# Kernel tuning notes

Measured on AMD Instinct MI355X. Metric: run time of the kernel, lower is better.

Reference implementation:

```python
import jax, jax.numpy as jnp
import numpy as np

B, T, H, OUT = 128, 1024, 256, 2


def setup_inputs() -> dict:
    key = jax.random.key(0)
    ks = jax.random.split(key, 16)
    s_in = 1.0 / np.sqrt(1 + H)
    s_2h = 1.0 / np.sqrt(2 * H)
    s_o = 1.0 / np.sqrt(H)
    return {
        "x": jax.random.normal(ks[0], (B, T, 2), dtype=jnp.float32),
        "h_0": jax.random.normal(ks[1], (1, B, H), dtype=jnp.float32) * 0.1,
        "Wa": jax.random.normal(ks[2], (1 + H, H), dtype=jnp.float32) * s_in,
        "ba": jnp.zeros((H,), dtype=jnp.float32),
        "Wp1": jax.random.normal(ks[3], (1 + H, H), dtype=jnp.float32) * s_in,
        "bp1": jnp.zeros((H,), dtype=jnp.float32),
        "Wp2": jax.random.normal(ks[4], (1 + H, H), dtype=jnp.float32) * s_in,
        "bp2": jnp.zeros((H,), dtype=jnp.float32),
        "Wz": jax.random.normal(ks[5], (2 * H, H), dtype=jnp.float32) * s_2h,
        "bz": jnp.zeros((H,), dtype=jnp.float32),
        "Wh": jax.random.normal(ks[6], (2 * H, H), dtype=jnp.float32) * s_2h,
        "bh": jnp.zeros((H,), dtype=jnp.float32),
        "Wo": jax.random.normal(ks[7], (H, OUT), dtype=jnp.float32) * s_o,
        "bo": jnp.zeros((OUT,), dtype=jnp.float32),
    }


def _pgjanet_scan(x, h0, Wa, ba, Wp1, bp1, Wp2, bp2, Wz, bz, Wh, bh):
    # x: [B, T, 2], h0: [B, H]
    xt_all = jnp.swapaxes(x, 0, 1)  # [T, B, 2]

    def step(h, xt):
        amp = xt[:, 0:1]                       # [B, 1]
        ph = xt[:, 1:2]                        # [B, 1]
        a = jnp.tanh(jnp.concatenate([amp, h], axis=-1) @ Wa + ba)
        p1 = jnp.tanh(jnp.concatenate([jnp.cos(ph), h], axis=-1) @ Wp1 + bp1)
        p2 = jnp.tanh(jnp.concatenate([jnp.sin(ph), h], axis=-1) @ Wp2 + bp2)
        u = a * p1 * p2 * (1 - a) * (1 - p1) * (1 - p2)
        newin = jnp.concatenate([u, h], axis=-1)  # [B, 2H]
        z = jax.nn.sigmoid(newin @ Wz + bz)
        h_cand = jnp.tanh(newin @ Wh + bh)
        h_new = z * h + (1 - z) * h_cand
        return h_new, h_new

    h_n, hs = jax.lax.scan(step, h0, xt_all)
    return jnp.swapaxes(hs, 0, 1), h_n  # [B, T, H], [B, H]


def reference(x, h_0, Wa, ba, Wp1, bp1, Wp2, bp2, Wz, bz, Wh, bh, Wo, bo):
    hs, h_n = _pgjanet_scan(x, h_0[0], Wa, ba, Wp1, bp1, Wp2, bp2, Wz, bz, Wh, bh)
    out = hs @ Wo + bo  # [B, T, OUT]
    return (out, h_n)
```

## Files before the change

kernel.cpp:

```cpp
#include <hip/hip_runtime.h>
#include <math.h>


#define B_   128
#define T_   1024
#define H_   256
#define GB   32
#define GC   8
#define MB   4
#define NS   32
#define NTHR 512
#define HP   260

typedef float    f32x4 __attribute__((ext_vector_type(4)));
typedef unsigned u32x4 __attribute__((ext_vector_type(4)));

__device__ __forceinline__ void sys_st_x4(unsigned* p, u32x4 v) {
  asm volatile("global_store_dwordx4 %0, %1, off sc0 sc1" :: "v"(p), "v"(v) : "memory");
}
__device__ __forceinline__ u32x4 sys_ld_x4(const unsigned* p) {
  u32x4 v;
  asm volatile("global_load_dwordx4 %0, %1, off sc0 sc1\n\ts_waitcnt vmcnt(0)"
               : "=v"(v) : "v"(p) : "memory");
  return v;
}

__launch_bounds__(NTHR, 1)
__global__ void pgjanet_persist(
    const float* __restrict__ x,   const float* __restrict__ h0,
    const float* __restrict__ Wa,  const float* __restrict__ ba,
    const float* __restrict__ Wp1, const float* __restrict__ bp1,
    const float* __restrict__ Wp2, const float* __restrict__ bp2,
    const float* __restrict__ Wz,  const float* __restrict__ bz,
    const float* __restrict__ Wh,  const float* __restrict__ bh,
    const float* __restrict__ Wo,  const float* __restrict__ bo,
    float* __restrict__ out,
    unsigned* __restrict__ u_ex,
    unsigned* __restrict__ h_ex)
{
  __shared__ __align__(16) float h_lds[MB][HP];
  __shared__ __align__(16) float u_lds[MB][HP];
  __shared__ __align__(16) float wo_s[H_ * 2];
  __shared__ __align__(16) float xin[2][MB][4];

  const int wg   = blockIdx.x;
  const int g    = wg >> 3;
  const int gc   = wg & 7;
  const int tid  = threadIdx.x;
  const int col  = tid >> 4;
  const int kk   = tid & 15;
  const int b0   = g * MB;
  const int colg = gc * NS + col;

  f32x4 w1r[3][4]; float w1r0_[3], b1_[3];
#pragma unroll
  for (int m = 0; m < 3; ++m) {
    const float* W  = (m == 0) ? Wa : (m == 1 ? Wp1 : Wp2);
    const float* bb = (m == 0) ? ba : (m == 1 ? bp1 : bp2);
#pragma unroll
    for (int j = 0; j < 4; ++j) {
      f32x4 w;
#pragma unroll
      for (int c = 0; c < 4; ++c)
        w[c] = W[(1 + kk * 4 + j * 64 + c) * H_ + colg];
      w1r[m][j] = w;
    }
    w1r0_[m] = W[colg];
    b1_[m]   = bb[colg];
  }
  f32x4 w2r[2][8];
#pragma unroll
  for (int m = 0; m < 2; ++m) {
    const float* W = (m == 0) ? Wz : Wh;
#pragma unroll
    for (int j = 0; j < 8; ++j) {
      int rb = (j < 4) ? (kk * 4 + j * 64) : (256 + kk * 4 + (j - 4) * 64);
      f32x4 w;
#pragma unroll
      for (int c = 0; c < 4; ++c)
        w[c] = W[(rb + c) * H_ + colg];
      w2r[m][j] = w;
    }
  }
  const float bz_c = bz[colg], bh_c = bh[colg];
  const float bo0 = bo[0], bo1 = bo[1];
  for (int i = tid; i < H_ * 2; i += NTHR) wo_s[i] = Wo[i];
  {
    int b = tid >> 7, c2 = (tid & 127) * 2;
    float2 hv = *(const float2*)(h0 + (size_t)(b0 + b) * H_ + c2);
    h_lds[b][c2] = hv.x; h_lds[b][c2 + 1] = hv.y;
  }
  if (tid < MB) {
    float2 xt = *(const float2*)(x + ((size_t)(b0 + tid) * T_) * 2);
    xin[0][tid][0] = xt.x; xin[0][tid][1] = cosf(xt.y);
    xin[0][tid][2] = sinf(xt.y); xin[0][tid][3] = 0.f;
  }
  __syncthreads();

  unsigned* u_exg = u_ex + g * 2048;
  unsigned* h_exg = h_ex + g * 2048;
  unsigned* u_my  = u_exg + (gc * 64 + (col >> 1) * 4) * 4;
  unsigned* h_my  = h_exg + (gc * 64 + (col >> 1) * 4) * 4;
  const unsigned* pu = u_exg + tid * 4;
  const unsigned* ph = h_exg + tid * 4;
  const int cpg = ((tid >> 6) * 16 + ((tid >> 2) & 15)) * 2;
  const int cb  = tid & 3;
  const int em  = kk >> 2, eb = kk & 3;

  for (int t = 0; t < T_; ++t) {
    const unsigned seq = (unsigned)(t + 1);
    const int xb = t & 1;

    float acc[12];
#pragma unroll
    for (int i = 0; i < 12; ++i) acc[i] = 0.f;
#pragma unroll
    for (int b = 0; b < MB; ++b) {
#pragma unroll
      for (int j = 0; j < 4; ++j) {
        f32x4 h4 = *(const f32x4*)&h_lds[b][kk * 4 + j * 64];
#pragma unroll
        for (int m = 0; m < 3; ++m) {
          float s = acc[m * 4 + b];
          s = fmaf(h4[0], w1r[m][j][0], s); s = fmaf(h4[1], w1r[m][j][1], s);
          s = fmaf(h4[2], w1r[m][j][2], s); s = fmaf(h4[3], w1r[m][j][3], s);
          acc[m * 4 + b] = s;
        }
      }
    }
#pragma unroll
    for (int i = 0; i < 12; ++i) {
      float v = acc[i];
      v += __shfl_xor(v, 1); v += __shfl_xor(v, 2);
      v += __shfl_xor(v, 4); v += __shfl_xor(v, 8);
      acc[i] = v;
    }
    {
      float pre1 = acc[0];
#pragma unroll
      for (int i = 1; i < 12; ++i) if (kk == i) pre1 = acc[i];
      float w0  = em == 0 ? w1r0_[0] : (em == 1 ? w1r0_[1] : w1r0_[2]);
      float bb1 = em == 0 ? b1_[0]   : (em == 1 ? b1_[1]   : b1_[2]);
      f32x4 xi4 = *(const f32x4*)&xin[xb][eb][0];
      float xim = em == 0 ? xi4[0] : (em == 1 ? xi4[1] : xi4[2]);
      float tv  = tanhf(pre1 + xim * w0 + bb1);
      float p1v = __shfl(tv, kk + 4, 16);
      float p2v = __shfl(tv, kk + 8, 16);
      float uv  = tv * p1v * p2v * (1.f - tv) * (1.f - p1v) * (1.f - p2v);
      float uodd = __shfl_xor(uv, 16);
      if (kk < 4 && !(col & 1)) {
        u32x4 ch;
        ch.x = __float_as_uint(uv); ch.y = __float_as_uint(uodd);
        ch.z = seq; ch.w = 0u;
        sys_st_x4(u_my + eb * 4, ch);
      }
    }

    float acc2[8];
#pragma unroll
    for (int i = 0; i < 8; ++i) acc2[i] = 0.f;
#pragma unroll
    for (int b = 0; b < MB; ++b) {
#pragma unroll
      for (int j = 0; j < 4; ++j) {
        f32x4 h4 = *(const f32x4*)&h_lds[b][kk * 4 + j * 64];
#pragma unroll
        for (int m = 0; m < 2; ++m) {
          float s = acc2[m * 4 + b];
          s = fmaf(h4[0], w2r[m][4 + j][0], s); s = fmaf(h4[1], w2r[m][4 + j][1], s);
          s = fmaf(h4[2], w2r[m][4 + j][2], s); s = fmaf(h4[3], w2r[m][4 + j][3], s);
          acc2[m * 4 + b] = s;
        }
      }
    }

    {
      u32x4 c;
      for (;;) {
        c = sys_ld_x4(pu);
        if (c.z == seq) break;
        __builtin_amdgcn_s_sleep(1);
      }
      float2 d; d.x = __uint_as_float(c.x); d.y = __uint_as_float(c.y);
      *(float2*)&u_lds[cb][cpg] = d;
    }
    __syncthreads();

#pragma unroll
    for (int b = 0; b < MB; ++b) {
#pragma unroll
      for (int j = 0; j < 4; ++j) {
        f32x4 u4 = *(const f32x4*)&u_lds[b][kk * 4 + j * 64];
#pragma unroll
        for (int m = 0; m < 2; ++m) {
          float s = acc2[m * 4 + b];
          s = fmaf(u4[0], w2r[m][j][0], s); s = fmaf(u4[1], w2r[m][j][1], s);
          s = fmaf(u4[2], w2r[m][j][2], s); s = fmaf(u4[3], w2r[m][j][3], s);
          acc2[m * 4 + b] = s;
        }
      }
    }
#pragma unroll
    for (int i = 0; i < 8; ++i) {
      float v = acc2[i];
      v += __shfl_xor(v, 1); v += __shfl_xor(v, 2);
      v += __shfl_xor(v, 4); v += __shfl_xor(v, 8);
      acc2[i] = v;
    }
    {
      float pre2 = acc2[0];
#pragma unroll
      for (int i = 1; i < 8; ++i) if (kk == i) pre2 = acc2[i];
      float v2 = pre2 + (em == 0 ? bz_c : bh_c);
      float gv;
      if (em == 0) gv = 1.f / (1.f + expf(-v2));
      else         gv = tanhf(v2);
      float hcv   = __shfl(gv, kk + 4, 16);
      float hprev = h_lds[eb][colg];
      float hn    = gv * hprev + (1.f - gv) * hcv;
      float hnodd = __shfl_xor(hn, 16);
      if (kk < 4 && !(col & 1)) {
        u32x4 ch;
        ch.x = __float_as_uint(hn); ch.y = __float_as_uint(hnodd);
        ch.z = seq; ch.w = 0u;
        sys_st_x4(h_my + eb * 4, ch);
      }
      if (t == T_ - 1 && kk < 4)
        out[(size_t)B_ * T_ * 2 + (size_t)(b0 + eb) * H_ + colg] = hn;
    }

    if (t > 0 && gc < MB && tid < 64) {
      f32x4 h4  = *(const f32x4*)&h_lds[gc][tid * 4];
      f32x4 wo0 = *(const f32x4*)&wo_s[tid * 8];
      f32x4 wo1 = *(const f32x4*)&wo_s[tid * 8 + 4];
      float v0 = h4[0] * wo0[0] + h4[1] * wo0[2] + h4[2] * wo1[0] + h4[3] * wo1[2];
      float v1 = h4[0] * wo0[1] + h4[1] * wo0[3] + h4[2] * wo1[1] + h4[3] * wo1[3];
      v0 += __shfl_xor(v0, 1);  v1 += __shfl_xor(v1, 1);
      v0 += __shfl_xor(v0, 2);  v1 += __shfl_xor(v1, 2);
      v0 += __shfl_xor(v0, 4);  v1 += __shfl_xor(v1, 4);
      v0 += __shfl_xor(v0, 8);  v1 += __shfl_xor(v1, 8);
      v0 += __shfl_xor(v0, 16); v1 += __shfl_xor(v1, 16);
      v0 += __shfl_xor(v0, 32); v1 += __shfl_xor(v1, 32);
      if (tid == 0) {
        float2 o; o.x = v0 + bo0; o.y = v1 + bo1;
        *(float2*)(out + ((size_t)(b0 + gc) * T_ + (t - 1)) * 2) = o;
      }
    }
    if (t + 1 < T_ && tid < MB) {
      float2 xt = *(const float2*)(x + ((size_t)(b0 + tid) * T_ + (t + 1)) * 2);
      xin[xb ^ 1][tid][0] = xt.x; xin[xb ^ 1][tid][1] = cosf(xt.y);
      xin[xb ^ 1][tid][2] = sinf(xt.y); xin[xb ^ 1][tid][3] = 0.f;
    }
    __syncthreads();

    {
      u32x4 c;
      for (;;) {
        c = sys_ld_x4(ph);
        if (c.z == seq) break;
        __builtin_amdgcn_s_sleep(1);
      }
      float2 d; d.x = __uint_as_float(c.x); d.y = __uint_as_float(c.y);
      *(float2*)&h_lds[cb][cpg] = d;
    }
    __syncthreads();
  }

  if (gc < MB && tid < 64) {
    f32x4 h4  = *(const f32x4*)&h_lds[gc][tid * 4];
    f32x4 wo0 = *(const f32x4*)&wo_s[tid * 8];
    f32x4 wo1 = *(const f32x4*)&wo_s[tid * 8 + 4];
    float v0 = h4[0] * wo0[0] + h4[1] * wo0[2] + h4[2] * wo1[0] + h4[3] * wo1[2];
    float v1 = h4[0] * wo0[1] + h4[1] * wo0[3] + h4[2] * wo1[1] + h4[3] * wo1[3];
    v0 += __shfl_xor(v0, 1);  v1 += __shfl_xor(v1, 1);
    v0 += __shfl_xor(v0, 2);  v1 += __shfl_xor(v1, 2);
    v0 += __shfl_xor(v0, 4);  v1 += __shfl_xor(v1, 4);
    v0 += __shfl_xor(v0, 8);  v1 += __shfl_xor(v1, 8);
    v0 += __shfl_xor(v0, 16); v1 += __shfl_xor(v1, 16);
    v0 += __shfl_xor(v0, 32); v1 += __shfl_xor(v1, 32);
    if (tid == 0) {
      float2 o; o.x = v0 + bo0; o.y = v1 + bo1;
      *(float2*)(out + ((size_t)(b0 + gc) * T_ + (T_ - 1)) * 2) = o;
    }
  }
}

extern "C" void kernel_launch(void* const* d_in, const int* in_sizes, int n_in,
                              void* d_out, int out_size, void* d_ws, size_t ws_size,
                              hipStream_t stream) {
  (void)in_sizes; (void)n_in; (void)out_size; (void)ws_size;
  const float* x   = (const float*)d_in[0];
  const float* h0  = (const float*)d_in[1];
  const float* Wa  = (const float*)d_in[2];
  const float* ba  = (const float*)d_in[3];
  const float* Wp1 = (const float*)d_in[4];
  const float* bp1 = (const float*)d_in[5];
  const float* Wp2 = (const float*)d_in[6];
  const float* bp2 = (const float*)d_in[7];
  const float* Wz  = (const float*)d_in[8];
  const float* bz  = (const float*)d_in[9];
  const float* Wh  = (const float*)d_in[10];
  const float* bh  = (const float*)d_in[11];
  const float* Wo  = (const float*)d_in[12];
  const float* bo  = (const float*)d_in[13];

  float* out = (float*)d_out;
  char*  ws  = (char*)d_ws;
  unsigned* u_ex = (unsigned*)ws;
  unsigned* h_ex = (unsigned*)(ws + 262144);

  hipMemsetAsync(ws, 0, 524288, stream);

  pgjanet_persist<<<dim3(GB * GC), dim3(NTHR), 0, stream>>>(
      x, h0, Wa, ba, Wp1, bp1, Wp2, bp2, Wz, bz, Wh, bh, Wo, bo,
      out, u_ex, h_ex);
}
```

Baseline: 6.948 ms.

## Repartition persistent GRU across 16 groups of 8 batches with 16 column-split blocks

```diff
diff --git a/kernel.cpp b/kernel.cpp
--- a/kernel.cpp
+++ b/kernel.cpp
@@ -5,12 +5,11 @@
 #define B_   128
 #define T_   1024
 #define H_   256
-#define GB   32
-#define GC   8
-#define MB   4
-#define NS   32
+#define GB   16
+#define GC   16
+#define MB   8
 #define NTHR 512
-#define HP   260
+#define HPAD 264
 
 typedef float    f32x4 __attribute__((ext_vector_type(4)));
 typedef unsigned u32x4 __attribute__((ext_vector_type(4)));
@@ -18,11 +17,12 @@
 __device__ __forceinline__ void sys_st_x4(unsigned* p, u32x4 v) {
   asm volatile("global_store_dwordx4 %0, %1, off sc0 sc1" :: "v"(p), "v"(v) : "memory");
 }
-__device__ __forceinline__ u32x4 sys_ld_x4(const unsigned* p) {
-  u32x4 v;
-  asm volatile("global_load_dwordx4 %0, %1, off sc0 sc1\n\ts_waitcnt vmcnt(0)"
-               : "=v"(v) : "v"(p) : "memory");
-  return v;
+__device__ __forceinline__ void sys_ld2_x4(const unsigned* p0, const unsigned* p1,
+                                           u32x4& a, u32x4& b) {
+  asm volatile("global_load_dwordx4 %0, %2, off sc0 sc1\n\t"
+               "global_load_dwordx4 %1, %3, off sc0 sc1\n\t"
+               "s_waitcnt vmcnt(0)"
+               : "=&v"(a), "=&v"(b) : "v"(p0), "v"(p1) : "memory");
 }
 
 __launch_bounds__(NTHR, 1)
@@ -38,19 +38,23 @@
     unsigned* __restrict__ u_ex,
     unsigned* __restrict__ h_ex)
 {
-  __shared__ __align__(16) float h_lds[MB][HP];
-  __shared__ __align__(16) float u_lds[MB][HP];
+  __shared__ __align__(16) float h_lds[MB * HPAD];
+  __shared__ __align__(16) float u_lds[MB * HPAD];
   __shared__ __align__(16) float wo_s[H_ * 2];
   __shared__ __align__(16) float xin[2][MB][4];
 
   const int wg   = blockIdx.x;
-  const int g    = wg >> 3;
-  const int gc   = wg & 7;
+  const int g    = wg >> 4;
+  const int gc   = wg & 15;
   const int tid  = threadIdx.x;
-  const int col  = tid >> 4;
-  const int kk   = tid & 15;
+  const int lane = tid & 63;
+  const int w    = tid >> 6;
+  const int kl   = lane & 15;
+  const int bhlf = (lane >> 4) & 1;
+  const int cp   = (lane >> 5) & 1;
+  const int col  = w * 2 + cp;
+  const int colg = gc * 16 + col;
   const int b0   = g * MB;
-  const int colg = gc * NS + col;
 
   f32x4 w1r[3][4]; float w1r0_[3], b1_[3];
 #pragma unroll
@@ -59,11 +63,11 @@
     const float* bb = (m == 0) ? ba : (m == 1 ? bp1 : bp2);
 #pragma unroll
     for (int j = 0; j < 4; ++j) {
-      f32x4 w;
+      f32x4 v;
 #pragma unroll
       for (int c = 0; c < 4; ++c)
-        w[c] = W[(1 + kk * 4 + j * 64 + c) * H_ + colg];
-      w1r[m][j] = w;
+        v[c] = W[(1 + kl * 4 + j * 64 + c) * H_ + colg];
+      w1r[m][j] = v;
     }
     w1r0_[m] = W[colg];
     b1_[m]   = bb[colg];
@@ -74,21 +78,21 @@
     const float* W = (m == 0) ? Wz : Wh;
 #pragma unroll
     for (int j = 0; j < 8; ++j) {
-      int rb = (j < 4) ? (kk * 4 + j * 64) : (256 + kk * 4 + (j - 4) * 64);
-      f32x4 w;
+      int rb = (j < 4) ? (kl * 4 + j * 64) : (256 + kl * 4 + (j - 4) * 64);
+      f32x4 v;
 #pragma unroll
       for (int c = 0; c < 4; ++c)
-        w[c] = W[(rb + c) * H_ + colg];
-      w2r[m][j] = w;
+        v[c] = W[(rb + c) * H_ + colg];
+      w2r[m][j] = v;
     }
   }
   const float bz_c = bz[colg], bh_c = bh[colg];
   const float bo0 = bo[0], bo1 = bo[1];
   for (int i = tid; i < H_ * 2; i += NTHR) wo_s[i] = Wo[i];
   {
-    int b = tid >> 7, c2 = (tid & 127) * 2;
-    float2 hv = *(const float2*)(h0 + (size_t)(b0 + b) * H_ + c2);
-    h_lds[b][c2] = hv.x; h_lds[b][c2 + 1] = hv.y;
+    int row = tid >> 6, k4 = (tid & 63) * 4;
+    *(f32x4*)&h_lds[row * HPAD + k4] =
+        *(const f32x4*)(h0 + (size_t)(b0 + row) * H_ + k4);
   }
   if (tid < MB) {
     float2 xt = *(const float2*)(x + ((size_t)(b0 + tid) * T_) * 2);
@@ -97,15 +101,14 @@
   }
   __syncthreads();
 
-  unsigned* u_exg = u_ex + g * 2048;
-  unsigned* h_exg = h_ex + g * 2048;
-  unsigned* u_my  = u_exg + (gc * 64 + (col >> 1) * 4) * 4;
-  unsigned* h_my  = h_exg + (gc * 64 + (col >> 1) * 4) * 4;
-  const unsigned* pu = u_exg + tid * 4;
-  const unsigned* ph = h_exg + tid * 4;
-  const int cpg = ((tid >> 6) * 16 + ((tid >> 2) & 15)) * 2;
-  const int cb  = tid & 3;
-  const int em  = kk >> 2, eb = kk & 3;
+  unsigned* u_exg = u_ex + g * 4096;
+  unsigned* h_exg = h_ex + g * 4096;
+  unsigned* u_my  = u_exg + ((gc * 8 + w) * 8) * 4;
+  unsigned* h_my  = h_exg + ((gc * 8 + w) * 8) * 4;
+  const unsigned* pu0 = u_exg + tid * 4;
+  const unsigned* pu1 = u_exg + (tid + 512) * 4;
+  const unsigned* ph0 = h_exg + tid * 4;
+  const unsigned* ph1 = h_exg + (tid + 512) * 4;
 
   for (int t = 0; t < T_; ++t) {
     const unsigned seq = (unsigned)(t + 1);
@@ -115,16 +118,17 @@
 #pragma unroll
     for (int i = 0; i < 12; ++i) acc[i] = 0.f;
 #pragma unroll
-    for (int b = 0; b < MB; ++b) {
+    for (int bb = 0; bb < 4; ++bb) {
+      const float* hr = &h_lds[(bhlf * 4 + bb) * HPAD];
 #pragma unroll
       for (int j = 0; j < 4; ++j) {
-        f32x4 h4 = *(const f32x4*)&h_lds[b][kk * 4 + j * 64];
+        f32x4 h4 = *(const f32x4*)(hr + kl * 4 + j * 64);
 #pragma unroll
         for (int m = 0; m < 3; ++m) {
-          float s = acc[m * 4 + b];
+          float s = acc[m * 4 + bb];
           s = fmaf(h4[0], w1r[m][j][0], s); s = fmaf(h4[1], w1r[m][j][1], s);
           s = fmaf(h4[2], w1r[m][j][2], s); s = fmaf(h4[3], w1r[m][j][3], s);
-          acc[m * 4 + b] = s;
+          acc[m * 4 + bb] = s;
         }
       }
     }
@@ -137,102 +141,40 @@
     }
     {
       float pre1 = acc[0];
-#pragma unroll
-      for (int i = 1; i < 12; ++i) if (kk == i) pre1 = acc[i];
-      float w0  = em == 0 ? w1r0_[0] : (em == 1 ? w1r0_[1] : w1r0_[2]);
-      float bb1 = em == 0 ? b1_[0]   : (em == 1 ? b1_[1]   : b1_[2]);
-      f32x4 xi4 = *(const f32x4*)&xin[xb][eb][0];
-      float xim = em == 0 ? xi4[0] : (em == 1 ? xi4[1] : xi4[2]);
+      pre1 = (kl == 1)  ? acc[1]  : pre1;  pre1 = (kl == 2)  ? acc[2]  : pre1;
+      pre1 = (kl == 3)  ? acc[3]  : pre1;  pre1 = (kl == 4)  ? acc[4]  : pre1;
+      pre1 = (kl == 5)  ? acc[5]  : pre1;  pre1 = (kl == 6)  ? acc[6]  : pre1;
+      pre1 = (kl == 7)  ? acc[7]  : pre1;  pre1 = (kl == 8)  ? acc[8]  : pre1;
+      pre1 = (kl == 9)  ? acc[9]  : pre1;  pre1 = (kl == 10) ? acc[10] : pre1;
+      pre1 = (kl == 11) ? acc[11] : pre1;
+      int m = kl >> 2;
+      int batch = bhlf * 4 + (kl & 3);
+      float w0  = (m == 0) ? w1r0_[0] : ((m == 1) ? w1r0_[1] : w1r0_[2]);
+      float bb1 = (m == 0) ? b1_[0]   : ((m == 1) ? b1_[1]   : b1_[2]);
+      float xam = xin[xb][batch][0], xcs = xin[xb][batch][1], xsn = xin[xb][batch][2];
+      float xim = (m == 0) ? xam : ((m == 1) ? xcs : xsn);
       float tv  = tanhf(pre1 + xim * w0 + bb1);
-      float p1v = __shfl(tv, kk + 4, 16);
-      float p2v = __shfl(tv, kk + 8, 16);
+      float p1v = __shfl(tv, kl + 4, 16);
+      float p2v = __shfl(tv, kl + 8, 16);
       float uv  = tv * p1v * p2v * (1.f - tv) * (1.f - p1v) * (1.f - p2v);
-      float uodd = __shfl_xor(uv, 16);
-      if (kk < 4 && !(col & 1)) {
+      float uodd = __shfl_xor(uv, 32);
+      if (lane < 32 && kl < 4) {
         u32x4 ch;
         ch.x = __float_as_uint(uv); ch.y = __float_as_uint(uodd);
         ch.z = seq; ch.w = 0u;
-        sys_st_x4(u_my + eb * 4, ch);
-      }
-    }
-
-    float acc2[8];
-#pragma unroll
-    for (int i = 0; i < 8; ++i) acc2[i] = 0.f;
-#pragma unroll
-    for (int b = 0; b < MB; ++b) {
-#pragma unroll
-      for (int j = 0; j < 4; ++j) {
-        f32x4 h4 = *(const f32x4*)&h_lds[b][kk * 4 + j * 64];
-#pragma unroll
-        for (int m = 0; m < 2; ++m) {
-          float s = acc2[m * 4 + b];
-          s = fmaf(h4[0], w2r[m][4 + j][0], s); s = fmaf(h4[1], w2r[m][4 + j][1], s);
-          s = fmaf(h4[2], w2r[m][4 + j][2], s); s = fmaf(h4[3], w2r[m][4 + j][3], s);
-          acc2[m * 4 + b] = s;
-        }
-      }
-    }
-
-    {
-      u32x4 c;
-      for (;;) {
-        c = sys_ld_x4(pu);
-        if (c.z == seq) break;
-        __builtin_amdgcn_s_sleep(1);
-      }
-      float2 d; d.x = __uint_as_float(c.x); d.y = __uint_as_float(c.y);
-      *(float2*)&u_lds[cb][cpg] = d;
-    }
-    __syncthreads();
-
-#pragma unroll
-    for (int b = 0; b < MB; ++b) {
-#pragma unroll
-      for (int j = 0; j < 4; ++j) {
-        f32x4 u4 = *(const f32x4*)&u_lds[b][kk * 4 + j * 64];
-#pragma unroll
-        for (int m = 0; m < 2; ++m) {
-          float s = acc2[m * 4 + b];
-          s = fmaf(u4[0], w2r[m][j][0], s); s = fmaf(u4[1], w2r[m][j][1], s);
-          s = fmaf(u4[2], w2r[m][j][2], s); s = fmaf(u4[3], w2r[m][j][3], s);
-          acc2[m * 4 + b] = s;
-        }
-      }
-    }
-#pragma unroll
-    for (int i = 0; i < 8; ++i) {
-      float v = acc2[i];
-      v += __shfl_xor(v, 1); v += __shfl_xor(v, 2);
-      v += __shfl_xor(v, 4); v += __shfl_xor(v, 8);
-      acc2[i] = v;
-    }
-    {
-      float pre2 = acc2[0];
-#pragma unroll
-      for (int i = 1; i < 8; ++i) if (kk == i) pre2 = acc2[i];
-      float v2 = pre2 + (em == 0 ? bz_c : bh_c);
-      float gv;
-      if (em == 0) gv = 1.f / (1.f + expf(-v2));
-      else         gv = tanhf(v2);
-      float hcv   = __shfl(gv, kk + 4, 16);
-      float hprev = h_lds[eb][colg];
-      float hn    = gv * hprev + (1.f - gv) * hcv;
-      float hnodd = __shfl_xor(hn, 16);
-      if (kk < 4 && !(col & 1)) {
-        u32x4 ch;
-        ch.x = __float_as_uint(hn); ch.y = __float_as_uint(hnodd);
-        ch.z = seq; ch.w = 0u;
-        sys_st_x4(h_my + eb * 4, ch);
-      }
-      if (t == T_ - 1 && kk < 4)
-        out[(size_t)B_ * T_ * 2 + (size_t)(b0 + eb) * H_ + colg] = hn;
-    }
-
-    if (t > 0 && gc < MB && tid < 64) {
-      f32x4 h4  = *(const f32x4*)&h_lds[gc][tid * 4];
-      f32x4 wo0 = *(const f32x4*)&wo_s[tid * 8];
-      f32x4 wo1 = *(const f32x4*)&wo_s[tid * 8 + 4];
+        sys_st_x4(u_my + (bhlf * 4 + kl) * 4, ch);
+      }
+    }
+
+    if (t + 1 < T_ && tid < MB) {
+      float2 xt = *(const float2*)(x + ((size_t)(b0 + tid) * T_ + (t + 1)) * 2);
+      xin[xb ^ 1][tid][0] = xt.x; xin[xb ^ 1][tid][1] = cosf(xt.y);
+      xin[xb ^ 1][tid][2] = sinf(xt.y); xin[xb ^ 1][tid][3] = 0.f;
+    }
+    if (t > 0 && ((t - 1) & 15) == gc) {
+      f32x4 h4  = *(const f32x4*)&h_lds[w * HPAD + lane * 4];
+      f32x4 wo0 = *(const f32x4*)&wo_s[lane * 8];
+      f32x4 wo1 = *(const f32x4*)&wo_s[lane * 8 + 4];
       float v0 = h4[0] * wo0[0] + h4[1] * wo0[2] + h4[2] * wo1[0] + h4[3] * wo1[2];
       float v1 = h4[0] * wo0[1] + h4[1] * wo0[3] + h4[2] * wo1[1] + h4[3] * wo1[3];
       v0 += __shfl_xor(v0, 1);  v1 += __shfl_xor(v1, 1);
@@ -241,35 +183,114 @@
       v0 += __shfl_xor(v0, 8);  v1 += __shfl_xor(v1, 8);
       v0 += __shfl_xor(v0, 16); v1 += __shfl_xor(v1, 16);
       v0 += __shfl_xor(v0, 32); v1 += __shfl_xor(v1, 32);
-      if (tid == 0) {
+      if (lane == 0) {
         float2 o; o.x = v0 + bo0; o.y = v1 + bo1;
-        *(float2*)(out + ((size_t)(b0 + gc) * T_ + (t - 1)) * 2) = o;
-      }
-    }
-    if (t + 1 < T_ && tid < MB) {
-      float2 xt = *(const float2*)(x + ((size_t)(b0 + tid) * T_ + (t + 1)) * 2);
-      xin[xb ^ 1][tid][0] = xt.x; xin[xb ^ 1][tid][1] = cosf(xt.y);
-      xin[xb ^ 1][tid][2] = sinf(xt.y); xin[xb ^ 1][tid][3] = 0.f;
+        *(float2*)(out + ((size_t)(b0 + w) * T_ + (t - 1)) * 2) = o;
+      }
+    }
+    float acc2[8];
+#pragma unroll
+    for (int i = 0; i < 8; ++i) acc2[i] = 0.f;
+#pragma unroll
+    for (int bb = 0; bb < 4; ++bb) {
+      const float* hr = &h_lds[(bhlf * 4 + bb) * HPAD];
+#pragma unroll
+      for (int j = 0; j < 4; ++j) {
+        f32x4 h4 = *(const f32x4*)(hr + kl * 4 + j * 64);
+#pragma unroll
+        for (int m = 0; m < 2; ++m) {
+          float s = acc2[m * 4 + bb];
+          s = fmaf(h4[0], w2r[m][4 + j][0], s); s = fmaf(h4[1], w2r[m][4 + j][1], s);
+          s = fmaf(h4[2], w2r[m][4 + j][2], s); s = fmaf(h4[3], w2r[m][4 + j][3], s);
+          acc2[m * 4 + bb] = s;
+        }
+      }
+    }
+
+    {
+      u32x4 A, Bc;
+      for (;;) {
+        sys_ld2_x4(pu0, pu1, A, Bc);
+        if (A.z == seq && Bc.z == seq) break;
+        __builtin_amdgcn_s_sleep(1);
+      }
+      int c = tid;
+      float2 d0; d0.x = __uint_as_float(A.x); d0.y = __uint_as_float(A.y);
+      *(float2*)&u_lds[(c & 7) * HPAD + (c >> 6) * 16 + ((c >> 3) & 7) * 2] = d0;
+      c = tid + 512;
+      float2 d1; d1.x = __uint_as_float(Bc.x); d1.y = __uint_as_float(Bc.y);
+      *(float2*)&u_lds[(c & 7) * HPAD + (c >> 6) * 16 + ((c >> 3) & 7) * 2] = d1;
     }
     __syncthreads();
 
+#pragma unroll
+    for (int bb = 0; bb < 4; ++bb) {
+      const float* ur = &u_lds[(bhlf * 4 + bb) * HPAD];
+#pragma unroll
+      for (int j = 0; j < 4; ++j) {
+        f32x4 u4 = *(const f32x4*)(ur + kl * 4 + j * 64);
+#pragma unroll
+        for (int m = 0; m < 2; ++m) {
+          float s = acc2[m * 4 + bb];
+          s = fmaf(u4[0], w2r[m][j][0], s); s = fmaf(u4[1], w2r[m][j][1], s);
+          s = fmaf(u4[2], w2r[m][j][2], s); s = fmaf(u4[3], w2r[m][j][3], s);
+          acc2[m * 4 + bb] = s;
+        }
+      }
+    }
+#pragma unroll
+    for (int i = 0; i < 8; ++i) {
+      float v = acc2[i];
+      v += __shfl_xor(v, 1); v += __shfl_xor(v, 2);
+      v += __shfl_xor(v, 4); v += __shfl_xor(v, 8);
+      acc2[i] = v;
+    }
     {
-      u32x4 c;
+      float pre2 = acc2[0];
+      pre2 = (kl == 1) ? acc2[1] : pre2;  pre2 = (kl == 2) ? acc2[2] : pre2;
+      pre2 = (kl == 3) ? acc2[3] : pre2;  pre2 = (kl == 4) ? acc2[4] : pre2;
+      pre2 = (kl == 5) ? acc2[5] : pre2;  pre2 = (kl == 6) ? acc2[6] : pre2;
+      pre2 = (kl == 7) ? acc2[7] : pre2;
+      int m = kl >> 2;
+      int batch = bhlf * 4 + (kl & 3);
+      float v2 = pre2 + ((m == 0) ? bz_c : bh_c);
+      float gv = (m == 0) ? (1.f / (1.f + expf(-v2))) : tanhf(v2);
+      float hcv   = __shfl(gv, kl + 4, 16);
+      float hprev = h_lds[batch * HPAD + colg];
+      float hn    = gv * hprev + (1.f - gv) * hcv;
+      float hnodd = __shfl_xor(hn, 32);
+      if (lane < 32 && kl < 4) {
+        u32x4 ch;
+        ch.x = __float_as_uint(hn); ch.y = __float_as_uint(hnodd);
+        ch.z = seq; ch.w = 0u;
+        sys_st_x4(h_my + (bhlf * 4 + kl) * 4, ch);
+      }
+      if (t == T_ - 1 && kl < 4)
+        out[(size_t)B_ * T_ * 2 + (size_t)(b0 + batch) * H_ + colg] = hn;
+    }
+    __syncthreads();
+
+    {
+      u32x4 A, Bc;
       for (;;) {
-        c = sys_ld_x4(ph);
-        if (c.z == seq) break;
+        sys_ld2_x4(ph0, ph1, A, Bc);
+        if (A.z == seq && Bc.z == seq) break;
         __builtin_amdgcn_s_sleep(1);
       }
-      float2 d; d.x = __uint_as_float(c.x); d.y = __uint_as_float(c.y);
-      *(float2*)&h_lds[cb][cpg] = d;
+      int c = tid;
+      float2 d0; d0.x = __uint_as_float(A.x); d0.y = __uint_as_float(A.y);
+      *(float2*)&h_lds[(c & 7) * HPAD + (c >> 6) * 16 + ((c >> 3) & 7) * 2] = d0;
+      c = tid + 512;
+      float2 d1; d1.x = __uint_as_float(Bc.x); d1.y = __uint_as_float(Bc.y);
+      *(float2*)&h_lds[(c & 7) * HPAD + (c >> 6) * 16 + ((c >> 3) & 7) * 2] = d1;
     }
     __syncthreads();
   }
 
-  if (gc < MB && tid < 64) {
-    f32x4 h4  = *(const f32x4*)&h_lds[gc][tid * 4];
-    f32x4 wo0 = *(const f32x4*)&wo_s[tid * 8];
-    f32x4 wo1 = *(const f32x4*)&wo_s[tid * 8 + 4];
+  if (gc == ((T_ - 1) & 15)) {
+    f32x4 h4  = *(const f32x4*)&h_lds[w * HPAD + lane * 4];
+    f32x4 wo0 = *(const f32x4*)&wo_s[lane * 8];
+    f32x4 wo1 = *(const f32x4*)&wo_s[lane * 8 + 4];
     float v0 = h4[0] * wo0[0] + h4[1] * wo0[2] + h4[2] * wo1[0] + h4[3] * wo1[2];
     float v1 = h4[0] * wo0[1] + h4[1] * wo0[3] + h4[2] * wo1[1] + h4[3] * wo1[3];
     v0 += __shfl_xor(v0, 1);  v1 += __shfl_xor(v1, 1);
@@ -278,9 +299,9 @@
     v0 += __shfl_xor(v0, 8);  v1 += __shfl_xor(v1, 8);
     v0 += __shfl_xor(v0, 16); v1 += __shfl_xor(v1, 16);
     v0 += __shfl_xor(v0, 32); v1 += __shfl_xor(v1, 32);
-    if (tid == 0) {
+    if (lane == 0) {
       float2 o; o.x = v0 + bo0; o.y = v1 + bo1;
-      *(float2*)(out + ((size_t)(b0 + gc) * T_ + (T_ - 1)) * 2) = o;
+      *(float2*)(out + ((size_t)(b0 + w) * T_ + (T_ - 1)) * 2) = o;
     }
   }
 }
```

Result: faster. 5.879 ms (-15.4%).
